# Performance work log

Hardware: AMD Instinct MI355X
Metric: run time of the kernel (lower is better)

## Reference

```python
import jax, jax.numpy as jnp
import numpy as np

N = 30000      # nodes
E = 240000     # edges (before self-loops)
D = 128        # vec_dim
L = 6          # GAT layers
NEG_SLOPE = 0.2
EPS = 1e-5


def setup_inputs() -> dict:
    key = jax.random.key(0)
    ks = jax.random.split(key, 20)
    s = 1.0 / np.sqrt(D)
    inp = {
        "x": jax.random.randint(ks[0], (N,), 0, 120),
        "edge_index": jax.random.randint(ks[1], (2, E), 0, N),
        "emb": jax.random.normal(ks[2], (120, D), jnp.float32) * 0.05,
        # stacked GATv2Conv params for 6 layers (heads=1)
        "Wl": jax.random.normal(ks[3], (L, D, D), jnp.float32) * s,
        "bl": jnp.zeros((L, D), jnp.float32),
        "Wr": jax.random.normal(ks[4], (L, D, D), jnp.float32) * s,
        "br": jnp.zeros((L, D), jnp.float32),
        "att": jax.random.normal(ks[5], (L, D), jnp.float32) * s,
        "conv_bias": jnp.zeros((L, D), jnp.float32),
        # PyG LayerNorm (applied after layers 0..4)
        "ln_g": jnp.ones((L - 1, D), jnp.float32),
        "ln_b": jnp.zeros((L - 1, D), jnp.float32),
        # outer Linear + BatchNorm1d
        "lin_W": jax.random.normal(ks[6], (D, D), jnp.float32) * s,
        "lin_b": jnp.zeros((D,), jnp.float32),
        "bn_g": jnp.ones((D,), jnp.float32),
        "bn_b": jnp.zeros((D,), jnp.float32),
    }
    return inp


def _segment_softmax(score, seg, num_segments):
    # numerically stable softmax over variable-degree neighborhoods
    m = jax.ops.segment_max(score, seg, num_segments=num_segments)
    ex = jnp.exp(score - m[seg])
    denom = jax.ops.segment_sum(ex, seg, num_segments=num_segments)
    return ex / denom[seg]


def _gat_forward(h, src, dst, Wl, bl, Wr, br, att, conv_bias, ln_g, ln_b):
    xg = h
    for i in range(L):
        xl = xg @ Wl[i] + bl[i]          # [N, D] source transform
        xr = xg @ Wr[i] + br[i]          # [N, D] target transform
        # GATv2 attention: a^T LeakyReLU(x_l[j] + x_r[i]) per edge j->i
        e = jax.nn.leaky_relu(xl[src] + xr[dst], NEG_SLOPE)   # [E2, D]
        score = e @ att[i]                                     # [E2]
        alpha = _segment_softmax(score, dst, N)                # [E2]
        msg = alpha[:, None] * xl[src]                         # [E2, D]
        xg = jax.ops.segment_sum(msg, dst, num_segments=N) + conv_bias[i]
        if i < L - 1:
            # PyG LayerNorm(mode='graph'): global mean/std, per-channel affine
            mu = xg.mean()
            var = ((xg - mu) ** 2).mean()
            xg = (xg - mu) / jnp.sqrt(var + EPS) * ln_g[i] + ln_b[i]
            xg = jax.nn.relu(xg)
            # dropout(0.1) is identity in eval mode
    return xg


def reference(x, edge_index, emb, Wl, bl, Wr, br, att, conv_bias,
              ln_g, ln_b, lin_W, lin_b, bn_g, bn_b):
    h = emb[x]                                      # [N, D]
    # PyG GATv2Conv default add_self_loops=True
    loops = jnp.arange(N, dtype=edge_index.dtype)
    src = jnp.concatenate([edge_index[0], loops])   # [E2]
    dst = jnp.concatenate([edge_index[1], loops])   # [E2]
    xg = _gat_forward(h, src, dst, Wl, bl, Wr, br, att, conv_bias, ln_g, ln_b)
    out = (h + xg) @ lin_W + lin_b                  # [N, D]
    # BatchNorm1d (batch-statistics / train-mode math)
    mu = out.mean(axis=0)
    var = out.var(axis=0)
    out = (out - mu) / jnp.sqrt(var + EPS) * bn_g + bn_b
    return out
```

## Files before the change

kernel.cpp:

```cpp
#include <hip/hip_runtime.h>
#include <math.h>

#define N_NODES 30000
#define N_EDGES 240000
#define E2 (N_EDGES + N_NODES)
#define D 128
#define LAYERS 6
#define NEG_SLOPE 0.2f
#define LN_EPS 1e-5f

typedef unsigned short u16;
typedef unsigned int u32;
using bfrag = __attribute__((ext_vector_type(8))) short;
using f32x4 = __attribute__((ext_vector_type(4))) float;

__device__ inline u16 f2bf(float f) {
    u32 u = __float_as_uint(f);
    u32 r = u + 0x7fffu + ((u >> 16) & 1u);
    return (u16)(r >> 16);
}
__device__ inline u32 pack2(float a, float b) { return (u32)f2bf(a) | ((u32)f2bf(b) << 16); }
__device__ inline float bflo(u32 u) { return __uint_as_float(u << 16); }
__device__ inline float bfhi(u32 u) { return __uint_as_float(u & 0xffff0000u); }
__device__ inline u32 bfadd2(u32 a, u32 b) {
    return pack2(bflo(a) + bflo(b), bfhi(a) + bfhi(b));
}

__global__ __launch_bounds__(256) void wt_convert(const float* __restrict__ Wl,
        const float* __restrict__ Wr, const float* __restrict__ linW, u16* __restrict__ wt)
{
    __shared__ u16 tile[128 * 129];
    int b = blockIdx.x;
    const float* src = (b == 12) ? linW
                     : ((b & 1) ? Wr + (size_t)(b >> 1) * 16384 : Wl + (size_t)(b >> 1) * 16384);
    int t = threadIdx.x;
    #pragma unroll 4
    for (int i = 0; i < 64; i++) {
        int idx = t + 256 * i;
        int k = idx >> 7, n = idx & 127;
        tile[n * 129 + k] = f2bf(src[idx]);
    }
    __syncthreads();
    u16* dst = wt + (size_t)b * 16384;
    #pragma unroll 4
    for (int i = 0; i < 64; i++) {
        int idx = t + 256 * i;
        int n = idx >> 7, k = idx & 127;
        dst[idx] = tile[n * 129 + k];
    }
}

__global__ __launch_bounds__(256) void embed_kernel(const int* __restrict__ x,
        const float* __restrict__ emb, u16* __restrict__ h_bf)
{
    int idx = blockIdx.x * 256 + threadIdx.x;
    if (idx >= N_NODES * 32) return;
    int n = idx >> 5, q = idx & 31;
    float4 v = ((const float4*)(emb + (size_t)x[n] * D))[q];
    ushort4 o;
    o.x = f2bf(v.x); o.y = f2bf(v.y); o.z = f2bf(v.z); o.w = f2bf(v.w);
    ((ushort4*)h_bf)[idx] = o;
}

__global__ __launch_bounds__(256) void hist_kernel(const int* __restrict__ ei, int* __restrict__ cnt)
{
    int e = blockIdx.x * 256 + threadIdx.x;
    if (e >= E2) return;
    int d = (e < N_EDGES) ? ei[N_EDGES + e] : (e - N_EDGES);
    atomicAdd(&cnt[d], 1);
}

__global__ __launch_bounds__(1024) void scan1_kernel(const int* __restrict__ cnt,
        int* __restrict__ lscan, int* __restrict__ bsum)
{
    __shared__ int wtot[16];
    int t = threadIdx.x, lane = t & 63, w = t >> 6;
    int i = blockIdx.x * 1024 + t;
    int v = (i < N_NODES) ? cnt[i] : 0;
    int s = v;
    #pragma unroll
    for (int off = 1; off < 64; off <<= 1) {
        int u = __shfl_up(s, off);
        if (lane >= off) s += u;
    }
    if (lane == 63) wtot[w] = s;
    __syncthreads();
    if (t < 16) {
        int xv = wtot[t];
        #pragma unroll
        for (int off = 1; off < 16; off <<= 1) {
            int u = __shfl_up(xv, off);
            if (t >= off) xv += u;
        }
        wtot[t] = xv;
    }
    __syncthreads();
    int incl = ((w == 0) ? 0 : wtot[w - 1]) + s;
    if (i < N_NODES) lscan[i] = incl;
    if (t == 0) bsum[blockIdx.x] = wtot[15];
}

__global__ __launch_bounds__(1024) void scan3_kernel(const int* __restrict__ lscan,
        const int* __restrict__ bsum, const int* __restrict__ cnt,
        int* __restrict__ row_off, int* __restrict__ cursor)
{
    __shared__ int sboff;
    if (threadIdx.x < 64) {
        int v = (threadIdx.x < 30) ? bsum[threadIdx.x] : 0;
        int s = v;
        #pragma unroll
        for (int off = 1; off < 64; off <<= 1) {
            int u = __shfl_up(s, off);
            if ((int)threadIdx.x >= off) s += u;
        }
        if (threadIdx.x == blockIdx.x) sboff = s - v;
    }
    __syncthreads();
    int i = blockIdx.x * 1024 + threadIdx.x;
    if (i == 0) row_off[0] = 0;
    if (i < N_NODES) {
        int r = lscan[i] + sboff;
        row_off[i + 1] = r;
        cursor[i] = r - cnt[i];
    }
}

__global__ __launch_bounds__(256) void scatter_kernel(const int* __restrict__ ei,
        int* __restrict__ cursor, int* __restrict__ csr_src)
{
    int e = blockIdx.x * 256 + threadIdx.x;
    if (e >= E2) return;
    int s, d;
    if (e < N_EDGES) { s = ei[e]; d = ei[N_EDGES + e]; }
    else             { s = e - N_EDGES; d = s; }
    int pos = atomicAdd(&cursor[d], 1);
    csr_src[pos] = s;
}

template<bool LN, bool DUAL, bool OUTF>
__global__ __launch_bounds__(256) void gemm_mfma(
    const u16* __restrict__ Abf, const u16* __restrict__ A2bf,
    const float* __restrict__ Aln, const float* __restrict__ lnacc,
    const float* __restrict__ lng, const float* __restrict__ lnb,
    const u16* __restrict__ Wt1, const float* __restrict__ b1,
    float* __restrict__ C1f, u16* __restrict__ C1h,
    const u16* __restrict__ Wt2, const float* __restrict__ b2, u16* __restrict__ C2h,
    int M)
{
    __shared__ u16 As[32 * 136];
    __shared__ float sLN[2];
    int t = threadIdx.x;
    int m0 = blockIdx.x * 32;
    int lane = t & 63, w = t >> 6;
    int n16 = lane & 15, quad = lane >> 4;
    int c0 = w * 32;

    bfrag bW1[2][4], bW2[2][4];
    #pragma unroll
    for (int c = 0; c < 2; c++)
        #pragma unroll
        for (int ks = 0; ks < 4; ks++)
            bW1[c][ks] = *(const bfrag*)(Wt1 + (size_t)(c0 + c * 16 + n16) * 128 + ks * 32 + quad * 8);
    if (DUAL) {
        #pragma unroll
        for (int c = 0; c < 2; c++)
            #pragma unroll
            for (int ks = 0; ks < 4; ks++)
                bW2[c][ks] = *(const bfrag*)(Wt2 + (size_t)(c0 + c * 16 + n16) * 128 + ks * 32 + quad * 8);
    }

    if (LN) {
        if (w == 0) {
            float2 v = ((const float2*)lnacc)[lane];
            float s = v.x, ss = v.y;
            #pragma unroll
            for (int off = 32; off > 0; off >>= 1) {
                s += __shfl_xor(s, off); ss += __shfl_xor(ss, off);
            }
            if (lane == 0) {
                const float invM = 1.f / ((float)N_NODES * (float)D);
                float mu  = s * invM;
                float var = ss * invM - mu * mu;
                sLN[0] = mu;
                sLN[1] = rsqrtf(var + LN_EPS);
            }
        }
        __syncthreads();
        float mu = sLN[0], inv = sLN[1];
        #pragma unroll
        for (int i = 0; i < 4; i++) {
            int idx = t + 256 * i;
            int row = idx >> 5, c4 = idx & 31;
            int gr = m0 + row;
            float4 v = make_float4(0.f, 0.f, 0.f, 0.f);
            if (gr < M) v = ((const float4*)(Aln + (size_t)gr * D))[c4];
            float4 gv = ((const float4*)lng)[c4];
            float4 bv = ((const float4*)lnb)[c4];
            v.x = (v.x - mu) * inv * gv.x + bv.x; v.x = v.x > 0.f ? v.x : 0.f;
            v.y = (v.y - mu) * inv * gv.y + bv.y; v.y = v.y > 0.f ? v.y : 0.f;
            v.z = (v.z - mu) * inv * gv.z + bv.z; v.z = v.z > 0.f ? v.z : 0.f;
            v.w = (v.w - mu) * inv * gv.w + bv.w; v.w = v.w > 0.f ? v.w : 0.f;
            uint2 pk = make_uint2(pack2(v.x, v.y), pack2(v.z, v.w));
            *(uint2*)&As[row * 136 + c4 * 4] = pk;
        }
    } else {
        #pragma unroll
        for (int i = 0; i < 2; i++) {
            int idx = t + 256 * i;
            int row = idx >> 4, c16 = idx & 15;
            int gr = m0 + row;
            uint4 v = make_uint4(0u, 0u, 0u, 0u);
            if (gr < M) {
                v = ((const uint4*)(Abf + (size_t)gr * 128))[c16];
                if (A2bf) {
                    uint4 u = ((const uint4*)(A2bf + (size_t)gr * 128))[c16];
                    v.x = bfadd2(v.x, u.x); v.y = bfadd2(v.y, u.y);
                    v.z = bfadd2(v.z, u.z); v.w = bfadd2(v.w, u.w);
                }
            }
            *(uint4*)&As[row * 136 + c16 * 8] = v;
        }
    }
    __syncthreads();

    f32x4 zero = {0.f, 0.f, 0.f, 0.f};
    f32x4 acc1[2][2] = {{zero, zero}, {zero, zero}};
    f32x4 acc2[2][2] = {{zero, zero}, {zero, zero}};
    #pragma unroll
    for (int ks = 0; ks < 4; ks++) {
        bfrag a[2];
        #pragma unroll
        for (int r = 0; r < 2; r++)
            a[r] = *(const bfrag*)&As[(r * 16 + n16) * 136 + ks * 32 + quad * 8];
        #pragma unroll
        for (int r = 0; r < 2; r++)
            #pragma unroll
            for (int c = 0; c < 2; c++) {
                acc1[r][c] = __builtin_amdgcn_mfma_f32_16x16x32_bf16(a[r], bW1[c][ks], acc1[r][c], 0, 0, 0);
                if (DUAL)
                    acc2[r][c] = __builtin_amdgcn_mfma_f32_16x16x32_bf16(a[r], bW2[c][ks], acc2[r][c], 0, 0, 0);
            }
    }

    float bv1[2] = { b1[c0 + n16], b1[c0 + 16 + n16] };
    #pragma unroll
    for (int r = 0; r < 2; r++)
        #pragma unroll
        for (int c = 0; c < 2; c++)
            #pragma unroll
            for (int reg = 0; reg < 4; reg++) {
                int grow = m0 + r * 16 + quad * 4 + reg;
                if (grow < M) {
                    float val = acc1[r][c][reg] + bv1[c];
                    int col = c0 + c * 16 + n16;
                    if (OUTF) C1f[(size_t)grow * 128 + col] = val;
                    else      C1h[(size_t)grow * 128 + col] = f2bf(val);
                }
            }
    if (DUAL) {
        float bv2[2] = { b2[c0 + n16], b2[c0 + 16 + n16] };
        #pragma unroll
        for (int r = 0; r < 2; r++)
            #pragma unroll
            for (int c = 0; c < 2; c++)
                #pragma unroll
                for (int reg = 0; reg < 4; reg++) {
                    int grow = m0 + r * 16 + quad * 4 + reg;
                    if (grow < M)
                        C2h[(size_t)grow * 128 + c0 + c * 16 + n16] = f2bf(acc2[r][c][reg] + bv2[c]);
                }
    }
}

__global__ __launch_bounds__(256) void gat_agg(
    const u16* __restrict__ xl, const u16* __restrict__ xr,
    const int* __restrict__ row_off, const int* __restrict__ csr_src,
    const float* __restrict__ att, const float* __restrict__ conv_bias,
    float* __restrict__ xg, u16* __restrict__ xg_bf, float* __restrict__ lnacc)
{
    __shared__ float stash[4][64][17];
    int wave = threadIdx.x >> 6, lane = threadIdx.x & 63;
    int node = blockIdx.x * 4 + wave;
    int g = lane >> 4, q = lane & 15;

    uint4 rr = *(const uint4*)(xr + (size_t)node * 128 + q * 8);
    float4 r0 = make_float4(bflo(rr.x), bfhi(rr.x), bflo(rr.y), bfhi(rr.y));
    float4 r1 = make_float4(bflo(rr.z), bfhi(rr.z), bflo(rr.w), bfhi(rr.w));
    float4 av0 = ((const float4*)att)[2 * q];
    float4 av1 = ((const float4*)att)[2 * q + 1];

    int s0 = row_off[node], s1 = row_off[node + 1];

    int base = blockIdx.x * 4;
    int cmax = 0;
    #pragma unroll
    for (int i = 0; i < 4; i++) {
        int d = row_off[base + i + 1] - row_off[base + i];
        int c = (d + 63) >> 6;
        cmax = c > cmax ? c : cmax;
    }

    float m = -3e38f, denom = 0.f;
    float4 a0 = make_float4(0.f, 0.f, 0.f, 0.f), a1 = a0;

    for (int ci = 0; ci < cmax; ci++) {
        int cs = s0 + ci * 64;
        int ce = cs + 64 < s1 ? cs + 64 : s1;
        int cnt = ce - cs; if (cnt < 0) cnt = 0;

        for (int s = cs + g; s < ce; s += 4) {
            int src = csr_src[s];
            uint4 raw = *(const uint4*)(xl + (size_t)src * 128 + q * 8);
            float4 v0 = make_float4(bflo(raw.x), bfhi(raw.x), bflo(raw.y), bfhi(raw.y));
            float4 v1 = make_float4(bflo(raw.z), bfhi(raw.z), bflo(raw.w), bfhi(raw.w));
            float pr = 0.f, tt;
            tt = v0.x + r0.x; tt = tt > 0.f ? tt : NEG_SLOPE * tt; pr += av0.x * tt;
            tt = v0.y + r0.y; tt = tt > 0.f ? tt : NEG_SLOPE * tt; pr += av0.y * tt;
            tt = v0.z + r0.z; tt = tt > 0.f ? tt : NEG_SLOPE * tt; pr += av0.z * tt;
            tt = v0.w + r0.w; tt = tt > 0.f ? tt : NEG_SLOPE * tt; pr += av0.w * tt;
            tt = v1.x + r1.x; tt = tt > 0.f ? tt : NEG_SLOPE * tt; pr += av1.x * tt;
            tt = v1.y + r1.y; tt = tt > 0.f ? tt : NEG_SLOPE * tt; pr += av1.y * tt;
            tt = v1.z + r1.z; tt = tt > 0.f ? tt : NEG_SLOPE * tt; pr += av1.z * tt;
            tt = v1.w + r1.w; tt = tt > 0.f ? tt : NEG_SLOPE * tt; pr += av1.w * tt;
            stash[wave][s - cs][q] = pr;
        }
        __syncthreads();

        float sc = -3e38f;
        if (lane < cnt) {
            float tsum = 0.f;
            #pragma unroll
            for (int j = 0; j < 16; j++) tsum += stash[wave][lane][j];
            sc = tsum;
        }
        float cm = sc;
        #pragma unroll
        for (int off = 32; off > 0; off >>= 1) cm = fmaxf(cm, __shfl_xor(cm, off));
        float mn = fmaxf(m, cm);
        float scale = __expf(m - mn);
        float wgt = (lane < cnt) ? __expf(sc - mn) : 0.f;
        float csum = wgt;
        #pragma unroll
        for (int off = 32; off > 0; off >>= 1) csum += __shfl_xor(csum, off);
        denom = denom * scale + csum;
        if (lane < cnt) stash[wave][lane][16] = wgt;
        __syncthreads();

        a0.x *= scale; a0.y *= scale; a0.z *= scale; a0.w *= scale;
        a1.x *= scale; a1.y *= scale; a1.z *= scale; a1.w *= scale;
        for (int s = cs + g; s < ce; s += 4) {
            float wv = stash[wave][s - cs][16];
            int src = csr_src[s];
            uint4 raw = *(const uint4*)(xl + (size_t)src * 128 + q * 8);
            a0.x += wv * bflo(raw.x); a0.y += wv * bfhi(raw.x);
            a0.z += wv * bflo(raw.y); a0.w += wv * bfhi(raw.y);
            a1.x += wv * bflo(raw.z); a1.y += wv * bfhi(raw.z);
            a1.z += wv * bflo(raw.w); a1.w += wv * bfhi(raw.w);
        }
        m = mn;
        __syncthreads();
    }

    #pragma unroll
    for (int msk = 16; msk <= 32; msk <<= 1) {
        a0.x += __shfl_xor(a0.x, msk); a0.y += __shfl_xor(a0.y, msk);
        a0.z += __shfl_xor(a0.z, msk); a0.w += __shfl_xor(a0.w, msk);
        a1.x += __shfl_xor(a1.x, msk); a1.y += __shfl_xor(a1.y, msk);
        a1.z += __shfl_xor(a1.z, msk); a1.w += __shfl_xor(a1.w, msk);
    }

    float4 cb0 = ((const float4*)conv_bias)[2 * q];
    float4 cb1 = ((const float4*)conv_bias)[2 * q + 1];
    float inv = 1.f / denom;
    float4 o0, o1;
    o0.x = a0.x * inv + cb0.x; o0.y = a0.y * inv + cb0.y;
    o0.z = a0.z * inv + cb0.z; o0.w = a0.w * inv + cb0.w;
    o1.x = a1.x * inv + cb1.x; o1.y = a1.y * inv + cb1.y;
    o1.z = a1.z * inv + cb1.z; o1.w = a1.w * inv + cb1.w;

    if (xg_bf) {
        if (g == 0) {
            uint4 pk = make_uint4(pack2(o0.x, o0.y), pack2(o0.z, o0.w),
                                  pack2(o1.x, o1.y), pack2(o1.z, o1.w));
            ((uint4*)(xg_bf + (size_t)node * 128))[q] = pk;
        }
    } else {
        if (g == 0) {
            ((float4*)(xg + (size_t)node * 128))[2 * q]     = o0;
            ((float4*)(xg + (size_t)node * 128))[2 * q + 1] = o1;
        }
        float s  = o0.x + o0.y + o0.z + o0.w + o1.x + o1.y + o1.z + o1.w;
        float ss = o0.x*o0.x + o0.y*o0.y + o0.z*o0.z + o0.w*o0.w
                 + o1.x*o1.x + o1.y*o1.y + o1.z*o1.z + o1.w*o1.w;
        #pragma unroll
        for (int off = 1; off < 16; off <<= 1) { s += __shfl_xor(s, off); ss += __shfl_xor(ss, off); }
        __shared__ float sred[8];
        if (lane == 0) { sred[wave] = s; sred[4 + wave] = ss; }
        __syncthreads();
        if (threadIdx.x == 0) {
            int slot = blockIdx.x & 63;
            atomicAdd(&lnacc[2 * slot],     sred[0] + sred[1] + sred[2] + sred[3]);
            atomicAdd(&lnacc[2 * slot + 1], sred[4] + sred[5] + sred[6] + sred[7]);
        }
    }
}

__global__ __launch_bounds__(256) void bn_reduce(const float* __restrict__ out, float* __restrict__ acc)
{
    int c = threadIdx.x & 127;
    int rg = threadIdx.x >> 7;
    float s = 0.f, ss = 0.f;
    for (int r = blockIdx.x * 2 + rg; r < N_NODES; r += gridDim.x * 2) {
        float v = out[(size_t)r * D + c];
        s += v; ss += v * v;
    }
    __shared__ float ls[256], lss[256];
    ls[threadIdx.x] = s; lss[threadIdx.x] = ss;
    __syncthreads();
    if (rg == 0) {
        s  = ls[c]  + ls[c + 128];
        ss = lss[c] + lss[c + 128];
        atomicAdd(&acc[c], s);
        atomicAdd(&acc[128 + c], ss);
    }
}

__global__ __launch_bounds__(256) void bn_apply(float* __restrict__ out, const float* __restrict__ acc,
        const float* __restrict__ g, const float* __restrict__ b)
{
    int idx = blockIdx.x * 256 + threadIdx.x;
    if (idx >= N_NODES * 32) return;
    int c4 = idx & 31;
    const float invN = 1.f / (float)N_NODES;
    float4 s1 = ((const float4*)(acc))[c4];
    float4 s2 = ((const float4*)(acc + 128))[c4];
    float4 gv = ((const float4*)g)[c4];
    float4 bv = ((const float4*)b)[c4];
    float4 v = ((float4*)out)[idx];
    float mu, var, inv;
    mu = s1.x * invN; var = s2.x * invN - mu * mu; inv = rsqrtf(var + LN_EPS);
    v.x = (v.x - mu) * inv * gv.x + bv.x;
    mu = s1.y * invN; var = s2.y * invN - mu * mu; inv = rsqrtf(var + LN_EPS);
    v.y = (v.y - mu) * inv * gv.y + bv.y;
    mu = s1.z * invN; var = s2.z * invN - mu * mu; inv = rsqrtf(var + LN_EPS);
    v.z = (v.z - mu) * inv * gv.z + bv.z;
    mu = s1.w * invN; var = s2.w * invN - mu * mu; inv = rsqrtf(var + LN_EPS);
    v.w = (v.w - mu) * inv * gv.w + bv.w;
    ((float4*)out)[idx] = v;
}

extern "C" void kernel_launch(void* const* d_in, const int* in_sizes, int n_in,
                              void* d_out, int out_size, void* d_ws, size_t ws_size,
                              hipStream_t stream)
{
    const int*   x    = (const int*)d_in[0];
    const int*   ei   = (const int*)d_in[1];
    const float* emb  = (const float*)d_in[2];
    const float* Wl   = (const float*)d_in[3];
    const float* bl   = (const float*)d_in[4];
    const float* Wr   = (const float*)d_in[5];
    const float* br   = (const float*)d_in[6];
    const float* att  = (const float*)d_in[7];
    const float* cbias= (const float*)d_in[8];
    const float* lng  = (const float*)d_in[9];
    const float* lnb  = (const float*)d_in[10];
    const float* linW = (const float*)d_in[11];
    const float* linb = (const float*)d_in[12];
    const float* bng  = (const float*)d_in[13];
    const float* bnb  = (const float*)d_in[14];
    float* out = (float*)d_out;

    char* p = (char*)d_ws;
    float* xg    = (float*)p; p += (size_t)N_NODES * D * 4;
    u16*   xl_bf = (u16*)p;   p += (size_t)N_NODES * D * 2;
    u16*   xr_bf = (u16*)p;   p += (size_t)N_NODES * D * 2;
    u16*   xg_bf = (u16*)p;   p += (size_t)N_NODES * D * 2;
    u16*   h_bf  = (u16*)p;   p += (size_t)N_NODES * D * 2;
    u16*   wt    = (u16*)p;   p += (size_t)13 * 16384 * 2;
    int* cnt     = (int*)p; p += ((N_NODES * 4 + 255) / 256) * 256;
    int* lscan   = (int*)p; p += ((N_NODES * 4 + 255) / 256) * 256;
    int* row_off = (int*)p; p += (((N_NODES + 1) * 4 + 255) / 256) * 256;
    int* cursor  = (int*)p; p += ((N_NODES * 4 + 255) / 256) * 256;
    int* csr_src = (int*)p; p += ((E2 * 4 + 255) / 256) * 256;
    int* bsum    = (int*)p; p += 256;
    float* accs  = (float*)p; p += 4096;

    hipMemsetAsync(cnt, 0, N_NODES * 4, stream);
    hipMemsetAsync(accs, 0, 4096, stream);

    wt_convert<<<13, 256, 0, stream>>>(Wl, Wr, linW, wt);
    embed_kernel<<<3750, 256, 0, stream>>>(x, emb, h_bf);
    hist_kernel<<<(E2 + 255) / 256, 256, 0, stream>>>(ei, cnt);
    scan1_kernel<<<30, 1024, 0, stream>>>(cnt, lscan, bsum);
    scan3_kernel<<<30, 1024, 0, stream>>>(lscan, bsum, cnt, row_off, cursor);
    scatter_kernel<<<(E2 + 255) / 256, 256, 0, stream>>>(ei, cursor, csr_src);

    for (int i = 0; i < LAYERS; i++) {
        if (i == 0) {
            gemm_mfma<false, true, false><<<938, 256, 0, stream>>>(
                h_bf, nullptr, nullptr, nullptr, nullptr, nullptr,
                wt + (size_t)0 * 16384, bl + 0, nullptr, xl_bf,
                wt + (size_t)1 * 16384, br + 0, xr_bf, N_NODES);
        } else {
            gemm_mfma<true, true, false><<<938, 256, 0, stream>>>(
                nullptr, nullptr, xg, accs + (i - 1) * 128,
                lng + (size_t)(i - 1) * D, lnb + (size_t)(i - 1) * D,
                wt + (size_t)(2 * i) * 16384, bl + i * D, nullptr, xl_bf,
                wt + (size_t)(2 * i + 1) * 16384, br + i * D, xr_bf, N_NODES);
        }
        gat_agg<<<7500, 256, 0, stream>>>(xl_bf, xr_bf, row_off, csr_src,
            att + i * D, cbias + i * D, xg,
            (i == LAYERS - 1) ? xg_bf : nullptr,
            (i < LAYERS - 1) ? (accs + i * 128) : nullptr);
    }
    gemm_mfma<false, false, true><<<938, 256, 0, stream>>>(
        xg_bf, h_bf, nullptr, nullptr, nullptr, nullptr,
        wt + (size_t)12 * 16384, linb, out, nullptr,
        nullptr, nullptr, nullptr, N_NODES);
    bn_reduce<<<256, 256, 0, stream>>>(out, accs + 640);
    bn_apply<<<3750, 256, 0, stream>>>(out, accs + 640, bng, bnb);
}
```

Measured before the change: 613.0 us.

## Fuse GATv2 score and aggregation into single pass without max-subtraction

```diff
diff --git a/kernel.cpp b/kernel.cpp
--- a/kernel.cpp
+++ b/kernel.cpp
@@ -278,7 +278,6 @@
     const float* __restrict__ att, const float* __restrict__ conv_bias,
     float* __restrict__ xg, u16* __restrict__ xg_bf, float* __restrict__ lnacc)
 {
-    __shared__ float stash[4][64][17];
     int wave = threadIdx.x >> 6, lane = threadIdx.x & 63;
     int node = blockIdx.x * 4 + wave;
     int g = lane >> 4, q = lane & 15;
@@ -290,79 +289,35 @@
     float4 av1 = ((const float4*)att)[2 * q + 1];
 
     int s0 = row_off[node], s1 = row_off[node + 1];
-
-    int base = blockIdx.x * 4;
-    int cmax = 0;
-    #pragma unroll
-    for (int i = 0; i < 4; i++) {
-        int d = row_off[base + i + 1] - row_off[base + i];
-        int c = (d + 63) >> 6;
-        cmax = c > cmax ? c : cmax;
-    }
-
-    float m = -3e38f, denom = 0.f;
+    float denom = 0.f;
     float4 a0 = make_float4(0.f, 0.f, 0.f, 0.f), a1 = a0;
 
-    for (int ci = 0; ci < cmax; ci++) {
-        int cs = s0 + ci * 64;
-        int ce = cs + 64 < s1 ? cs + 64 : s1;
-        int cnt = ce - cs; if (cnt < 0) cnt = 0;
-
-        for (int s = cs + g; s < ce; s += 4) {
-            int src = csr_src[s];
-            uint4 raw = *(const uint4*)(xl + (size_t)src * 128 + q * 8);
-            float4 v0 = make_float4(bflo(raw.x), bfhi(raw.x), bflo(raw.y), bfhi(raw.y));
-            float4 v1 = make_float4(bflo(raw.z), bfhi(raw.z), bflo(raw.w), bfhi(raw.w));
-            float pr = 0.f, tt;
-            tt = v0.x + r0.x; tt = tt > 0.f ? tt : NEG_SLOPE * tt; pr += av0.x * tt;
-            tt = v0.y + r0.y; tt = tt > 0.f ? tt : NEG_SLOPE * tt; pr += av0.y * tt;
-            tt = v0.z + r0.z; tt = tt > 0.f ? tt : NEG_SLOPE * tt; pr += av0.z * tt;
-            tt = v0.w + r0.w; tt = tt > 0.f ? tt : NEG_SLOPE * tt; pr += av0.w * tt;
-            tt = v1.x + r1.x; tt = tt > 0.f ? tt : NEG_SLOPE * tt; pr += av1.x * tt;
-            tt = v1.y + r1.y; tt = tt > 0.f ? tt : NEG_SLOPE * tt; pr += av1.y * tt;
-            tt = v1.z + r1.z; tt = tt > 0.f ? tt : NEG_SLOPE * tt; pr += av1.z * tt;
-            tt = v1.w + r1.w; tt = tt > 0.f ? tt : NEG_SLOPE * tt; pr += av1.w * tt;
-            stash[wave][s - cs][q] = pr;
-        }
-        __syncthreads();
-
-        float sc = -3e38f;
-        if (lane < cnt) {
-            float tsum = 0.f;
-            #pragma unroll
-            for (int j = 0; j < 16; j++) tsum += stash[wave][lane][j];
-            sc = tsum;
-        }
-        float cm = sc;
-        #pragma unroll
-        for (int off = 32; off > 0; off >>= 1) cm = fmaxf(cm, __shfl_xor(cm, off));
-        float mn = fmaxf(m, cm);
-        float scale = __expf(m - mn);
-        float wgt = (lane < cnt) ? __expf(sc - mn) : 0.f;
-        float csum = wgt;
-        #pragma unroll
-        for (int off = 32; off > 0; off >>= 1) csum += __shfl_xor(csum, off);
-        denom = denom * scale + csum;
-        if (lane < cnt) stash[wave][lane][16] = wgt;
-        __syncthreads();
-
-        a0.x *= scale; a0.y *= scale; a0.z *= scale; a0.w *= scale;
-        a1.x *= scale; a1.y *= scale; a1.z *= scale; a1.w *= scale;
-        for (int s = cs + g; s < ce; s += 4) {
-            float wv = stash[wave][s - cs][16];
-            int src = csr_src[s];
-            uint4 raw = *(const uint4*)(xl + (size_t)src * 128 + q * 8);
-            a0.x += wv * bflo(raw.x); a0.y += wv * bfhi(raw.x);
-            a0.z += wv * bflo(raw.y); a0.w += wv * bfhi(raw.y);
-            a1.x += wv * bflo(raw.z); a1.y += wv * bfhi(raw.z);
-            a1.z += wv * bflo(raw.w); a1.w += wv * bfhi(raw.w);
-        }
-        m = mn;
-        __syncthreads();
+    #pragma unroll 2
+    for (int s = s0 + g; s < s1; s += 4) {
+        int src = csr_src[s];
+        uint4 raw = *(const uint4*)(xl + (size_t)src * 128 + q * 8);
+        float4 v0 = make_float4(bflo(raw.x), bfhi(raw.x), bflo(raw.y), bfhi(raw.y));
+        float4 v1 = make_float4(bflo(raw.z), bfhi(raw.z), bflo(raw.w), bfhi(raw.w));
+        float pr = 0.f, tt;
+        tt = v0.x + r0.x; tt = tt > 0.f ? tt : NEG_SLOPE * tt; pr += av0.x * tt;
+        tt = v0.y + r0.y; tt = tt > 0.f ? tt : NEG_SLOPE * tt; pr += av0.y * tt;
+        tt = v0.z + r0.z; tt = tt > 0.f ? tt : NEG_SLOPE * tt; pr += av0.z * tt;
+        tt = v0.w + r0.w; tt = tt > 0.f ? tt : NEG_SLOPE * tt; pr += av0.w * tt;
+        tt = v1.x + r1.x; tt = tt > 0.f ? tt : NEG_SLOPE * tt; pr += av1.x * tt;
+        tt = v1.y + r1.y; tt = tt > 0.f ? tt : NEG_SLOPE * tt; pr += av1.y * tt;
+        tt = v1.z + r1.z; tt = tt > 0.f ? tt : NEG_SLOPE * tt; pr += av1.z * tt;
+        tt = v1.w + r1.w; tt = tt > 0.f ? tt : NEG_SLOPE * tt; pr += av1.w * tt;
+        #pragma unroll
+        for (int off = 1; off < 16; off <<= 1) pr += __shfl_xor(pr, off);
+        float wv = __expf(pr);
+        denom += wv;
+        a0.x += wv * v0.x; a0.y += wv * v0.y; a0.z += wv * v0.z; a0.w += wv * v0.w;
+        a1.x += wv * v1.x; a1.y += wv * v1.y; a1.z += wv * v1.z; a1.w += wv * v1.w;
     }
 
     #pragma unroll
     for (int msk = 16; msk <= 32; msk <<= 1) {
+        denom += __shfl_xor(denom, msk);
         a0.x += __shfl_xor(a0.x, msk); a0.y += __shfl_xor(a0.y, msk);
         a0.z += __shfl_xor(a0.z, msk); a0.w += __shfl_xor(a0.w, msk);
         a1.x += __shfl_xor(a1.x, msk); a1.y += __shfl_xor(a1.y, msk);
```

New measurement: 582.3 us. -5.0%, faster.
